# Kernel tuning notes

Hardware: AMD Instinct MI355X
Metric: run time of the kernel (lower is better)

The kernel has to match this reference:

```python
import jax, jax.numpy as jnp
import numpy as np

B, NQ, D, NH, DH = 16, 300, 256, 8, 32
L, P, FFN = 3, 4, 1024
LEVEL_SHAPES = [(80, 80), (40, 40), (20, 20)]
S = sum(h * w for h, w in LEVEL_SHAPES)  # 8400
EPS = 1e-5

PARAM_NAMES = ['wq', 'bq', 'wk', 'bk', 'wv', 'bv', 'wo', 'bo', 'ln1_g', 'ln1_b',
               'w_off', 'b_off', 'w_aw', 'b_aw', 'w_val', 'b_val', 'w_out', 'b_out',
               'ln2_g', 'ln2_b', 'w_fc1', 'b_fc1', 'w_fc2', 'b_fc2', 'ln3_g', 'ln3_b']


def _ln(x, g, b):
    m = jnp.mean(x, -1, keepdims=True)
    v = jnp.mean(jnp.square(x - m), -1, keepdims=True)
    return (x - m) * jax.lax.rsqrt(v + EPS) * g + b


def _bilinear(v_l, loc, Hl, Wl):
    # v_l: [B, Hl*Wl, NH, DH]; loc in [0,1]: [B, NQ, NH, P, 2]
    # matches torch grid_sample(align_corners=False, padding='zeros') with grid=2*loc-1
    x = loc[..., 0] * Wl - 0.5
    y = loc[..., 1] * Hl - 0.5
    x0 = jnp.floor(x)
    y0 = jnp.floor(y)
    vt = v_l.transpose(0, 2, 1, 3)  # [B, NH, Sl, DH]
    out = jnp.zeros((v_l.shape[0], NQ, NH, P, DH), v_l.dtype)
    for dx in (0, 1):
        for dy in (0, 1):
            xi = x0 + dx
            yi = y0 + dy
            w = (1.0 - jnp.abs(x - xi)) * (1.0 - jnp.abs(y - yi))
            valid = (xi >= 0) & (xi < Wl) & (yi >= 0) & (yi < Hl)
            idx = (jnp.clip(yi, 0, Hl - 1) * Wl + jnp.clip(xi, 0, Wl - 1)).astype(jnp.int32)
            idx_t = idx.transpose(0, 2, 1, 3).reshape(idx.shape[0], NH, NQ * P)
            g = jnp.take_along_axis(vt, idx_t[..., None], axis=2)  # [B, NH, NQ*P, DH]
            g = g.reshape(-1, NH, NQ, P, DH).transpose(0, 2, 1, 3, 4)
            out = out + g * (w * valid)[..., None]
    return out  # [B, NQ, NH, P, DH]


def _forward(hidden_states, pos_embed, encoder_hidden_states, reference_points, spatial_shapes, p):
    h = hidden_states
    # ---- self-attention (pos added to q and k only) ----
    hp = h + pos_embed
    q = (hp @ p['wq'] + p['bq']).reshape(B, NQ, NH, DH)
    k = (hp @ p['wk'] + p['bk']).reshape(B, NQ, NH, DH)
    v = (h @ p['wv'] + p['bv']).reshape(B, NQ, NH, DH)
    scores = jnp.einsum('bqhd,bkhd->bhqk', q, k) * (1.0 / np.sqrt(DH).astype(np.float32))
    attn = jax.nn.softmax(scores, -1)
    sa = jnp.einsum('bhqk,bkhd->bqhd', attn, v).reshape(B, NQ, D) @ p['wo'] + p['bo']
    h = _ln(h + sa, p['ln1_g'], p['ln1_b'])

    # ---- multiscale deformable cross-attention ----
    hp = h + pos_embed
    value = (encoder_hidden_states @ p['w_val'] + p['b_val']).reshape(B, S, NH, DH)
    off = (hp @ p['w_off'] + p['b_off']).reshape(B, NQ, NH, L, P, 2)
    aw = jax.nn.softmax((hp @ p['w_aw'] + p['b_aw']).reshape(B, NQ, NH, L * P), -1)
    aw = aw.reshape(B, NQ, NH, L, P)
    normalizer = jnp.stack([spatial_shapes[:, 1], spatial_shapes[:, 0]], -1).astype(h.dtype)  # [L,2] = (W,H)
    loc = reference_points[:, :, None, :, None, :] + off / normalizer[None, None, None, :, None, :]
    out = jnp.zeros((B, NQ, NH, DH), h.dtype)
    start = 0
    for l, (Hl, Wl) in enumerate(LEVEL_SHAPES):
        v_l = value[:, start:start + Hl * Wl]
        sampled = _bilinear(v_l, loc[:, :, :, l], Hl, Wl)  # [B,NQ,NH,P,DH]
        out = out + jnp.sum(sampled * aw[:, :, :, l, :, None], axis=3)
        start += Hl * Wl
    ca = out.reshape(B, NQ, D) @ p['w_out'] + p['b_out']
    h = _ln(h + ca, p['ln2_g'], p['ln2_b'])

    # ---- MLP ----
    mlp = jax.nn.relu(h @ p['w_fc1'] + p['b_fc1']) @ p['w_fc2'] + p['b_fc2']
    return _ln(h + mlp, p['ln3_g'], p['ln3_b'])


def setup_inputs() -> dict:
    key = jax.random.key(0)
    ks = iter(jax.random.split(key, 48))
    def nrm(shape, s=0.02):
        return jax.random.normal(next(ks), shape, jnp.float32) * s
    inp = {
        'hidden_states': jax.random.normal(next(ks), (B, NQ, D), jnp.float32),
        'pos_embed': jax.random.normal(next(ks), (B, NQ, D), jnp.float32),
        'encoder_hidden_states': jax.random.normal(next(ks), (B, S, D), jnp.float32),
        'reference_points': jax.random.uniform(next(ks), (B, NQ, L, 2), jnp.float32),
        'spatial_shapes': jnp.array(LEVEL_SHAPES, jnp.int32),
        'wq': nrm((D, D)), 'bq': jnp.zeros(D),
        'wk': nrm((D, D)), 'bk': jnp.zeros(D),
        'wv': nrm((D, D)), 'bv': jnp.zeros(D),
        'wo': nrm((D, D)), 'bo': jnp.zeros(D),
        'ln1_g': jnp.ones(D), 'ln1_b': jnp.zeros(D),
        'w_off': nrm((D, NH * L * P * 2)), 'b_off': nrm((NH * L * P * 2,), 0.1),
        'w_aw': nrm((D, NH * L * P)), 'b_aw': jnp.zeros(NH * L * P),
        'w_val': nrm((D, D)), 'b_val': jnp.zeros(D),
        'w_out': nrm((D, D)), 'b_out': jnp.zeros(D),
        'ln2_g': jnp.ones(D), 'ln2_b': jnp.zeros(D),
        'w_fc1': nrm((D, FFN)), 'b_fc1': jnp.zeros(FFN),
        'w_fc2': nrm((FFN, D)), 'b_fc2': jnp.zeros(D),
        'ln3_g': jnp.ones(D), 'ln3_b': jnp.zeros(D),
    }
    return inp


def reference(hidden_states, pos_embed, encoder_hidden_states, reference_points, spatial_shapes,
              wq, bq, wk, bk, wv, bv, wo, bo, ln1_g, ln1_b,
              w_off, b_off, w_aw, b_aw, w_val, b_val, w_out, b_out,
              ln2_g, ln2_b, w_fc1, b_fc1, w_fc2, b_fc2, ln3_g, ln3_b):
    p = dict(wq=wq, bq=bq, wk=wk, bk=bk, wv=wv, bv=bv, wo=wo, bo=bo,
             ln1_g=ln1_g, ln1_b=ln1_b, w_off=w_off, b_off=b_off, w_aw=w_aw, b_aw=b_aw,
             w_val=w_val, b_val=b_val, w_out=w_out, b_out=b_out, ln2_g=ln2_g, ln2_b=ln2_b,
             w_fc1=w_fc1, b_fc1=b_fc1, w_fc2=w_fc2, b_fc2=b_fc2, ln3_g=ln3_g, ln3_b=ln3_b)
    return _forward(hidden_states, pos_embed, encoder_hidden_states, reference_points, spatial_shapes, p)
```

## Files before the change

### kernel.cpp

```cpp
#include <hip/hip_runtime.h>
#include <hip/hip_bf16.h>
#include <math.h>

#define B_   16
#define NQ_  300
#define D_   256
#define NH_  8
#define DH_  32
#define L_   3
#define P_   4
#define FFN_ 1024
#define S_   8400
#define ROWS_ (B_*NQ_)
#define NB_   (ROWS_*D_)

typedef __attribute__((ext_vector_type(4))) unsigned short ushort4_t;
typedef __attribute__((ext_vector_type(8))) unsigned short ushort8_t;
typedef __attribute__((ext_vector_type(8))) short bf16x8;
typedef __attribute__((ext_vector_type(4))) float f32x4;

__device__ inline unsigned short f2b(float f) {
    __hip_bfloat16 h = __float2bfloat16(f);
    return __builtin_bit_cast(unsigned short, h);
}
__device__ inline float b2f(unsigned short u) {
    union { unsigned u; float f; } c; c.u = ((unsigned)u) << 16; return c.f;
}

__global__ __launch_bounds__(256) void prep_kernel(
    const float* __restrict__ wq, const float* __restrict__ wk,
    const float* __restrict__ wv, const float* __restrict__ wo,
    const float* __restrict__ w_val, const float* __restrict__ w_out,
    const float* __restrict__ w_off, const float* __restrict__ w_aw,
    const float* __restrict__ w_fc1, const float* __restrict__ w_fc2,
    const float* __restrict__ bq, const float* __restrict__ bk,
    const float* __restrict__ b_off, const float* __restrict__ b_aw,
    unsigned short* __restrict__ wtqk, unsigned short* __restrict__ wtv,
    unsigned short* __restrict__ wto, unsigned short* __restrict__ wtval,
    unsigned short* __restrict__ wtout, unsigned short* __restrict__ wtoa,
    unsigned short* __restrict__ wtfc1, unsigned short* __restrict__ wtfc2,
    float* __restrict__ bqk, float* __restrict__ boa)
{
    const int bid = blockIdx.x;
    if (bid >= 968) {
        int idx = (bid - 968)*256 + threadIdx.x;
        if (idx < 512) bqk[idx] = (idx < 256) ? bq[idx] : bk[idx-256];
        else { int j = idx - 512; if (j < 288) boa[j] = (j < 192) ? b_off[j] : b_aw[j-192]; }
        return;
    }
    const float* src; unsigned short* dst; int K, N, t;
    if      (bid < 64)  { src=wq;    dst=wtqk;         K=256;  N=256;  t=bid; }
    else if (bid < 128) { src=wk;    dst=wtqk+65536;   K=256;  N=256;  t=bid-64; }
    else if (bid < 192) { src=wv;    dst=wtv;          K=256;  N=256;  t=bid-128; }
    else if (bid < 256) { src=wo;    dst=wto;          K=256;  N=256;  t=bid-192; }
    else if (bid < 320) { src=w_val; dst=wtval;        K=256;  N=256;  t=bid-256; }
    else if (bid < 384) { src=w_out; dst=wtout;        K=256;  N=256;  t=bid-320; }
    else if (bid < 432) { src=w_off; dst=wtoa;         K=256;  N=192;  t=bid-384; }
    else if (bid < 456) { src=w_aw;  dst=wtoa+49152;   K=256;  N=96;   t=bid-432; }
    else if (bid < 712) { src=w_fc1; dst=wtfc1;        K=256;  N=1024; t=bid-456; }
    else                { src=w_fc2; dst=wtfc2;        K=1024; N=256;  t=bid-712; }

    __shared__ unsigned short tl[32][33];
    int tid = threadIdx.x;
    int tx = tid & 31, ty = tid >> 5;
    int ntx = N >> 5;
    int n0 = (t % ntx) * 32, k0 = (t / ntx) * 32;
    #pragma unroll
    for (int i = 0; i < 4; ++i)
        tl[tx][ty + i*8] = f2b(src[(size_t)(k0 + ty + i*8)*N + n0 + tx]);
    __syncthreads();
    #pragma unroll
    for (int i = 0; i < 4; ++i)
        dst[(size_t)(n0 + ty + i*8)*K + k0 + tx] = tl[ty + i*8][tx];
}

#define GEMM_PREAMBLE()                                                        \
    const int tid  = threadIdx.x;                                              \
    const int lane = tid & 63;                                                 \
    const int w    = tid >> 6;                                                 \
    const int wr   = w >> 1, wc = w & 1;                                       \
    const int m0   = blockIdx.y * 64;                                          \
    const int n0   = blockIdx.x * 128;                                         \
    const int fr   = lane & 15, fq = lane >> 4;                                \
    const int arow = tid >> 2, aseg = (tid & 3) * 8;                           \
    const int brow = tid >> 1, bseg = (tid & 1) * 16;                          \
    const bool a_ok = (m0 + arow) < M;                                         \
    const bool b_ok = (n0 + brow) < N;                                         \
    const float*          aptr  = A  + (size_t)(m0 + arow)*K + aseg;           \
    const float*          aptr2 = A2 ? A2 + (size_t)(m0 + arow)*K + aseg : (const float*)0; \
    const unsigned short* bptr  = WT + (size_t)(n0 + brow)*K + bseg;           \
    f32x4 acc[2][4];                                                           \
    _Pragma("unroll") for (int m = 0; m < 2; ++m)                              \
        _Pragma("unroll") for (int n = 0; n < 4; ++n)                          \
            acc[m][n] = (f32x4){0.f, 0.f, 0.f, 0.f};                           \
    float4 avA0, avB0, avA1, avB1;                                             \
    ushort8_t bvA0, bvB0, bvA1, bvB1;

#define GEMM_LOAD(avA, avB, bvA, bvB, kk) do {                                 \
    if (a_ok) {                                                                \
        avA = *(const float4*)(aptr + (kk));                                   \
        avB = *(const float4*)(aptr + (kk) + 4);                               \
        if (aptr2) {                                                           \
            float4 x2 = *(const float4*)(aptr2 + (kk));                        \
            float4 y2 = *(const float4*)(aptr2 + (kk) + 4);                    \
            avA.x += x2.x; avA.y += x2.y; avA.z += x2.z; avA.w += x2.w;        \
            avB.x += y2.x; avB.y += y2.y; avB.z += y2.z; avB.w += y2.w;        \
        }                                                                      \
    } else { avA = (float4){0,0,0,0}; avB = (float4){0,0,0,0}; }               \
    if (b_ok) { bvA = *(const ushort8_t*)(bptr + (kk));                        \
                bvB = *(const ushort8_t*)(bptr + (kk) + 8); }                  \
    else { _Pragma("unroll") for (int j = 0; j < 8; ++j){bvA[j]=0;bvB[j]=0;} } \
} while (0)

#define GEMM_STORE_LDS(avA, avB, bvA, bvB) do {                                \
    ushort8_t ac;                                                              \
    ac[0]=f2b(avA.x); ac[1]=f2b(avA.y); ac[2]=f2b(avA.z); ac[3]=f2b(avA.w);    \
    ac[4]=f2b(avB.x); ac[5]=f2b(avB.y); ac[6]=f2b(avB.z); ac[7]=f2b(avB.w);    \
    *(ushort8_t*)&As[arow][aseg]     = ac;                                     \
    *(ushort8_t*)&Bs[brow][bseg]     = bvA;                                    \
    *(ushort8_t*)&Bs[brow][bseg + 8] = bvB;                                    \
} while (0)

#define GEMM_COMPUTE() do {                                                    \
    bf16x8 af[2], bfv[4];                                                      \
    _Pragma("unroll") for (int m = 0; m < 2; ++m)                              \
        af[m] = *(const bf16x8*)&As[wr*32 + m*16 + fr][fq*8];                  \
    _Pragma("unroll") for (int n = 0; n < 4; ++n)                              \
        bfv[n] = *(const bf16x8*)&Bs[wc*64 + n*16 + fr][fq*8];                 \
    _Pragma("unroll") for (int m = 0; m < 2; ++m)                              \
        _Pragma("unroll") for (int n = 0; n < 4; ++n)                          \
            acc[m][n] = __builtin_amdgcn_mfma_f32_16x16x32_bf16(               \
                af[m], bfv[n], acc[m][n], 0, 0, 0);                            \
} while (0)

#define GEMM_KLOOP()                                                           \
    GEMM_LOAD(avA0, avB0, bvA0, bvB0, 0);                                      \
    for (int k0 = 0; k0 < K; k0 += 64) {                                       \
        __syncthreads();                                                       \
        GEMM_STORE_LDS(avA0, avB0, bvA0, bvB0);                                \
        GEMM_LOAD(avA1, avB1, bvA1, bvB1, k0 + 32);                            \
        __syncthreads();                                                       \
        GEMM_COMPUTE();                                                        \
        __syncthreads();                                                       \
        GEMM_STORE_LDS(avA1, avB1, bvA1, bvB1);                                \
        if (k0 + 64 < K) GEMM_LOAD(avA0, avB0, bvA0, bvB0, k0 + 64);           \
        __syncthreads();                                                       \
        GEMM_COMPUTE();                                                        \
    }

__global__ __launch_bounds__(256) void gemm_mfma64(
    const float* __restrict__ A, const float* __restrict__ A2,
    const unsigned short* __restrict__ WT,
    const float* __restrict__ bias, float* __restrict__ C,
    int M, int N, int K, int relu)
{
    __shared__ unsigned short As[64][40];
    __shared__ unsigned short Bs[128][40];
    GEMM_PREAMBLE();
    GEMM_KLOOP();

    #pragma unroll
    for (int n = 0; n < 4; ++n) {
        int col = n0 + wc*64 + n*16 + fr;
        if (col < N) {
            float bcol = bias[col];
            #pragma unroll
            for (int m = 0; m < 2; ++m) {
                int rbase = m0 + wr*32 + m*16 + fq*4;
                #pragma unroll
                for (int r = 0; r < 4; ++r) {
                    int row = rbase + r;
                    if (row < M) {
                        float vv = acc[m][n][r] + bcol;
                        if (relu) vv = fmaxf(vv, 0.f);
                        C[(size_t)row * N + col] = vv;
                    }
                }
            }
        }
    }
}

__global__ __launch_bounds__(256) void stage1_kernel(
    const float* __restrict__ ehs, const float* __restrict__ h_in,
    const float* __restrict__ pos,
    const unsigned short* __restrict__ wtval, const float* __restrict__ b_val,
    unsigned short* __restrict__ val_bf,
    const unsigned short* __restrict__ wtqk, const float* __restrict__ bqk,
    float* __restrict__ buf_qk,
    const unsigned short* __restrict__ wtv, const float* __restrict__ bv,
    float* __restrict__ buf_v)
{
    __shared__ unsigned short As[64][40];
    __shared__ unsigned short Bs[128][40];

    const int bid = blockIdx.x;
    int path, m0, n0, Ncols = 256;
    const float* Ap; const float* A2p = nullptr;
    const unsigned short* Bp; const float* bias; float* C = nullptr;
    if (bid < 4200) {
        path = 0; m0 = (bid >> 1)*64; n0 = (bid & 1)*128;
        Ap = ehs; Bp = wtval; bias = b_val;
    } else if (bid < 4500) {
        int t = bid - 4200;
        path = 1; m0 = (t >> 2)*64; n0 = (t & 3)*128;
        Ap = h_in; A2p = pos; Bp = wtqk; bias = bqk; C = buf_qk; Ncols = 512;
    } else {
        int t = bid - 4500;
        path = 2; m0 = (t >> 1)*64; n0 = (t & 1)*128;
        Ap = h_in; Bp = wtv; bias = bv; C = buf_v;
    }

    const int tid  = threadIdx.x;
    const int lane = tid & 63;
    const int w    = tid >> 6;
    const int wr   = w >> 1, wc = w & 1;
    const int fr   = lane & 15, fq = lane >> 4;
    const int arow = tid >> 2, aseg = (tid & 3) * 8;
    const int brow = tid >> 1, bseg = (tid & 1) * 16;
    const bool a_ok = true, b_ok = true;
    const int K = 256;
    const float*          aptr  = Ap + (size_t)(m0 + arow)*256 + aseg;
    const float*          aptr2 = A2p ? A2p + (size_t)(m0 + arow)*256 + aseg : (const float*)0;
    const unsigned short* bptr  = Bp + (size_t)(n0 + brow)*256 + bseg;

    f32x4 acc[2][4];
    #pragma unroll
    for (int m = 0; m < 2; ++m)
        #pragma unroll
        for (int n = 0; n < 4; ++n)
            acc[m][n] = (f32x4){0.f, 0.f, 0.f, 0.f};
    float4 avA0, avB0, avA1, avB1;
    ushort8_t bvA0, bvB0, bvA1, bvB1;

    GEMM_KLOOP();

    if (path == 0) {
        #pragma unroll
        for (int n = 0; n < 4; ++n) {
            int col = n0 + wc*64 + n*16 + fr;
            int hh = col >> 5, dd = col & 31;
            float bcol = bias[col];
            #pragma unroll
            for (int m = 0; m < 2; ++m) {
                int rbase = m0 + wr*32 + m*16 + fq*4;
                #pragma unroll
                for (int r = 0; r < 4; ++r) {
                    unsigned row = rbase + r;
                    unsigned bb = row / (unsigned)S_;
                    unsigned ss = row - bb * (unsigned)S_;
                    val_bf[((size_t)(bb*NH_ + hh)*S_ + ss)*DH_ + dd] = f2b(acc[m][n][r] + bcol);
                }
            }
        }
    } else {
        #pragma unroll
        for (int n = 0; n < 4; ++n) {
            int col = n0 + wc*64 + n*16 + fr;
            float bcol = bias[col];
            #pragma unroll
            for (int m = 0; m < 2; ++m) {
                int rbase = m0 + wr*32 + m*16 + fq*4;
                #pragma unroll
                for (int r = 0; r < 4; ++r)
                    C[(size_t)(rbase + r) * Ncols + col] = acc[m][n][r] + bcol;
            }
        }
    }
}

__global__ __launch_bounds__(256) void gemm_relu_bf16(
    const float* __restrict__ A, const unsigned short* __restrict__ WT,
    const float* __restrict__ bias, unsigned short* __restrict__ OUT,
    int M, int N, int K)
{
    __shared__ unsigned short As[64][40];
    __shared__ unsigned short Bs[128][40];
    const float* A2 = nullptr;
    GEMM_PREAMBLE();
    GEMM_KLOOP();

    #pragma unroll
    for (int n = 0; n < 4; ++n) {
        int col = n0 + wc*64 + n*16 + fr;
        float bcol = bias[col];
        #pragma unroll
        for (int m = 0; m < 2; ++m) {
            int rbase = m0 + wr*32 + m*16 + fq*4;
            #pragma unroll
            for (int r = 0; r < 4; ++r)
                OUT[(size_t)(rbase + r) * N + col] = f2b(fmaxf(acc[m][n][r] + bcol, 0.f));
        }
    }
}

#define GLN_COMPUTE()  do {                                                    \
    bf16x8 af[2], bfv[8];                                                      \
    _Pragma("unroll") for (int m = 0; m < 2; ++m)                              \
        af[m] = *(const bf16x8*)&As[wr*32 + m*16 + fr][fq*8];                  \
    _Pragma("unroll") for (int n = 0; n < 8; ++n)                              \
        bfv[n] = *(const bf16x8*)&Bs[wc*128 + n*16 + fr][fq*8];                \
    _Pragma("unroll") for (int m = 0; m < 2; ++m)                              \
        _Pragma("unroll") for (int n = 0; n < 8; ++n)                          \
            acc[m][n] = __builtin_amdgcn_mfma_f32_16x16x32_bf16(               \
                af[m], bfv[n], acc[m][n], 0, 0, 0);                            \
} while (0)

#define GLN_EPILOGUE()                                                         \
    float gcol[8], bcol2[8], biascol[8];                                       \
    _Pragma("unroll") for (int n = 0; n < 8; ++n) {                            \
        int col = wc*128 + n*16 + fr;                                          \
        biascol[n] = bias[col]; gcol[n] = g[col]; bcol2[n] = bb[col];          \
    }                                                                          \
    _Pragma("unroll") for (int m = 0; m < 2; ++m) {                            \
        _Pragma("unroll") for (int r = 0; r < 4; ++r) {                        \
            int lrow = wr*32 + m*16 + fq*4 + r;                                \
            float s = 0.f, sq = 0.f;                                           \
            _Pragma("unroll") for (int n = 0; n < 8; ++n) {                    \
                float vv = acc[m][n][r] + biascol[n]                           \
                         + X[(size_t)(m0 + lrow)*256 + wc*128 + n*16 + fr];    \
                acc[m][n][r] = vv; s += vv; sq += vv*vv;                       \
            }                                                                  \
            s  += __shfl_xor(s, 1);  sq += __shfl_xor(sq, 1);                  \
            s  += __shfl_xor(s, 2);  sq += __shfl_xor(sq, 2);                  \
            s  += __shfl_xor(s, 4);  sq += __shfl_xor(sq, 4);                  \
            s  += __shfl_xor(s, 8);  sq += __shfl_xor(sq, 8);                  \
            if (fr == 0) { psum[lrow][wc] = s; psq[lrow][wc] = sq; }           \
        }                                                                      \
    }                                                                          \
    __syncthreads();                                                           \
    _Pragma("unroll") for (int m = 0; m < 2; ++m) {                            \
        _Pragma("unroll") for (int r = 0; r < 4; ++r) {                        \
            int lrow = wr*32 + m*16 + fq*4 + r;                                \
            float mean = (psum[lrow][0] + psum[lrow][1]) * (1.0f/256.0f);      \
            float ex2  = (psq[lrow][0]  + psq[lrow][1])  * (1.0f/256.0f);      \
            float rstd = rsqrtf(ex2 - mean*mean + 1e-5f);                      \
            _Pragma("unroll") for (int n = 0; n < 8; ++n) {                    \
                int col = wc*128 + n*16 + fr;                                  \
                OUT[(size_t)(m0 + lrow)*256 + col] =                           \
                    (acc[m][n][r] - mean)*rstd*gcol[n] + bcol2[n];             \
            }                                                                  \
        }                                                                      \
    }

__global__ __launch_bounds__(256) void gemm_ln_f32A(
    const float* __restrict__ A, const unsigned short* __restrict__ WT,
    const float* __restrict__ bias, const float* __restrict__ X,
    const float* __restrict__ g, const float* __restrict__ bb,
    float* __restrict__ OUT, int K)
{
    __shared__ unsigned short As[64][40];
    __shared__ unsigned short Bs[256][40];
    __shared__ float psum[64][2], psq[64][2];

    const int tid  = threadIdx.x;
    const int lane = tid & 63;
    const int w    = tid >> 6;
    const int wr   = w >> 1, wc = w & 1;
    const int m0   = blockIdx.x * 64;
    const int fr   = lane & 15, fq = lane >> 4;
    const int arow = tid >> 2, aseg = (tid & 3) * 8;
    const float*          aptr = A  + (size_t)(m0 + arow)*K + aseg;
    const unsigned short* bptr = WT + (size_t)tid*K;

    f32x4 acc[2][8];
    #pragma unroll
    for (int m = 0; m < 2; ++m)
        #pragma unroll
        for (int n = 0; n < 8; ++n)
            acc[m][n] = (f32x4){0.f, 0.f, 0.f, 0.f};

    float4 a0x, a0y, a1x, a1y;
    ushort8_t b0[4], b1[4];

    a0x = *(const float4*)(aptr); a0y = *(const float4*)(aptr + 4);
    #pragma unroll
    for (int j = 0; j < 4; ++j) b0[j] = *(const ushort8_t*)(bptr + j*8);
    for (int k0 = 0; k0 < K; k0 += 64) {
        __syncthreads();
        {
            ushort8_t ac;
            ac[0]=f2b(a0x.x); ac[1]=f2b(a0x.y); ac[2]=f2b(a0x.z); ac[3]=f2b(a0x.w);
            ac[4]=f2b(a0y.x); ac[5]=f2b(a0y.y); ac[6]=f2b(a0y.z); ac[7]=f2b(a0y.w);
            *(ushort8_t*)&As[arow][aseg] = ac;
            #pragma unroll
            for (int j = 0; j < 4; ++j) *(ushort8_t*)&Bs[tid][j*8] = b0[j];
        }
        a1x = *(const float4*)(aptr + k0 + 32); a1y = *(const float4*)(aptr + k0 + 36);
        #pragma unroll
        for (int j = 0; j < 4; ++j) b1[j] = *(const ushort8_t*)(bptr + k0 + 32 + j*8);
        __syncthreads();
        GLN_COMPUTE();
        __syncthreads();
        {
            ushort8_t ac;
            ac[0]=f2b(a1x.x); ac[1]=f2b(a1x.y); ac[2]=f2b(a1x.z); ac[3]=f2b(a1x.w);
            ac[4]=f2b(a1y.x); ac[5]=f2b(a1y.y); ac[6]=f2b(a1y.z); ac[7]=f2b(a1y.w);
            *(ushort8_t*)&As[arow][aseg] = ac;
            #pragma unroll
            for (int j = 0; j < 4; ++j) *(ushort8_t*)&Bs[tid][j*8] = b1[j];
        }
        if (k0 + 64 < K) {
            a0x = *(const float4*)(aptr + k0 + 64); a0y = *(const float4*)(aptr + k0 + 68);
            #pragma unroll
            for (int j = 0; j < 4; ++j) b0[j] = *(const ushort8_t*)(bptr + k0 + 64 + j*8);
        }
        __syncthreads();
        GLN_COMPUTE();
    }

    GLN_EPILOGUE();
}

__global__ __launch_bounds__(256) void gemm_ln_bf16A(
    const unsigned short* __restrict__ A, const unsigned short* __restrict__ WT,
    const float* __restrict__ bias, const float* __restrict__ X,
    const float* __restrict__ g, const float* __restrict__ bb,
    float* __restrict__ OUT, int K)
{
    __shared__ unsigned short As[64][40];
    __shared__ unsigned short Bs[256][40];
    __shared__ float psum[64][2], psq[64][2];

    const int tid  = threadIdx.x;
    const int lane = tid & 63;
    const int w    = tid >> 6;
    const int wr   = w >> 1, wc = w & 1;
    const int m0   = blockIdx.x * 64;
    const int fr   = lane & 15, fq = lane >> 4;
    const int arow = tid >> 2, aseg = (tid & 3) * 8;
    const unsigned short* aptr = A  + (size_t)(m0 + arow)*K + aseg;
    const unsigned short* bptr = WT + (size_t)tid*K;

    f32x4 acc[2][8];
    #pragma unroll
    for (int m = 0; m < 2; ++m)
        #pragma unroll
        for (int n = 0; n < 8; ++n)
            acc[m][n] = (f32x4){0.f, 0.f, 0.f, 0.f};

    ushort8_t a0, a1, b0[4], b1[4];

    a0 = *(const ushort8_t*)(aptr);
    #pragma unroll
    for (int j = 0; j < 4; ++j) b0[j] = *(const ushort8_t*)(bptr + j*8);
    for (int k0 = 0; k0 < K; k0 += 64) {
        __syncthreads();
        *(ushort8_t*)&As[arow][aseg] = a0;
        #pragma unroll
        for (int j = 0; j < 4; ++j) *(ushort8_t*)&Bs[tid][j*8] = b0[j];
        a1 = *(const ushort8_t*)(aptr + k0 + 32);
        #pragma unroll
        for (int j = 0; j < 4; ++j) b1[j] = *(const ushort8_t*)(bptr + k0 + 32 + j*8);
        __syncthreads();
        GLN_COMPUTE();
        __syncthreads();
        *(ushort8_t*)&As[arow][aseg] = a1;
        #pragma unroll
        for (int j = 0; j < 4; ++j) *(ushort8_t*)&Bs[tid][j*8] = b1[j];
        if (k0 + 64 < K) {
            a0 = *(const ushort8_t*)(aptr + k0 + 64);
            #pragma unroll
            for (int j = 0; j < 4; ++j) b0[j] = *(const ushort8_t*)(bptr + k0 + 64 + j*8);
        }
        __syncthreads();
        GLN_COMPUTE();
    }

    GLN_EPILOGUE();
}

__global__ __launch_bounds__(256) void self_attn_kernel(
    const float* __restrict__ qk, const float* __restrict__ v,
    float* __restrict__ sa)
{
    __shared__ unsigned short k_sw[304*32];
    __shared__ unsigned short vt[32][312];
    __shared__ unsigned short p_all[4][16][312];

    const int bid  = blockIdx.x;
    const int part = bid % 5;
    const int bh   = bid / 5;
    const int h    = bh & 7;
    const int b    = bh >> 3;
    const int tid  = threadIdx.x;
    const int lane = tid & 63;
    const int w    = tid >> 6;
    const int g    = lane >> 4;
    const int fr   = lane & 15;

    const size_t qbase = (size_t)b*NQ_*512 + h*DH_;
    const size_t kbase = qbase + 256;
    const size_t vbase = (size_t)b*NQ_*D_ + h*DH_;
    const size_t sbase = (size_t)b*NQ_*D_ + h*DH_;

    for (int i = tid; i < 1216; i += 256) {
        int r = i >> 2, u = i & 3;
        ushort8_t kb;
        if (r < NQ_) {
            const float* p8 = qk + kbase + (size_t)r*512 + u*8;
            float4 a0 = *(const float4*)p8;
            float4 a1 = *(const float4*)(p8 + 4);
            kb[0]=f2b(a0.x); kb[1]=f2b(a0.y); kb[2]=f2b(a0.z); kb[3]=f2b(a0.w);
            kb[4]=f2b(a1.x); kb[5]=f2b(a1.y); kb[6]=f2b(a1.z); kb[7]=f2b(a1.w);
        } else {
            #pragma unroll
            for (int j = 0; j < 8; ++j) kb[j] = 0;
        }
        int su = u ^ ((r >> 1) & 3);
        *(ushort8_t*)&k_sw[r*32 + su*8] = kb;
    }
    for (int i = tid; i < 1216; i += 256) {
        int kk = i >> 2, u = i & 3;
        if (kk < NQ_) {
            const float* p8 = v + vbase + (size_t)kk*D_ + u*8;
            float4 a0 = *(const float4*)p8;
            float4 a1 = *(const float4*)(p8 + 4);
            float f[8] = {a0.x,a0.y,a0.z,a0.w,a1.x,a1.y,a1.z,a1.w};
            #pragma unroll
            for (int j = 0; j < 8; ++j) vt[u*8 + j][kk] = f2b(f[j]);
        } else {
            #pragma unroll
            for (int j = 0; j < 8; ++j) vt[u*8 + j][kk] = 0;
        }
    }
    __syncthreads();

    const int q0 = part*64 + w*16;
    const int qi = q0 + fr;
    bf16x8 qf;
    if (qi < NQ_) {
        const float scale = 0.17677669529663687f;
        const float* p8 = qk + qbase + (size_t)qi*512 + g*8;
        float4 a0 = *(const float4*)p8;
        float4 a1 = *(const float4*)(p8 + 4);
        qf[0]=(short)f2b(a0.x*scale); qf[1]=(short)f2b(a0.y*scale);
        qf[2]=(short)f2b(a0.z*scale); qf[3]=(short)f2b(a0.w*scale);
        qf[4]=(short)f2b(a1.x*scale); qf[5]=(short)f2b(a1.y*scale);
        qf[6]=(short)f2b(a1.z*scale); qf[7]=(short)f2b(a1.w*scale);
    } else {
        #pragma unroll
        for (int j = 0; j < 8; ++j) qf[j] = 0;
    }

    const int ksw_u = g ^ ((fr >> 1) & 3);
    f32x4 acc[19];
    #pragma unroll
    for (int t = 0; t < 19; ++t) acc[t] = (f32x4){0.f,0.f,0.f,0.f};
    #pragma unroll
    for (int t = 0; t < 19; ++t) {
        int row = t*16 + fr;
        bf16x8 kf = *(const bf16x8*)&k_sw[row*32 + ksw_u*8];
        acc[t] = __builtin_amdgcn_mfma_f32_16x16x32_bf16(kf, qf, acc[t], 0, 0, 0);
    }
    if (g == 3) acc[18] = (f32x4){-1e30f, -1e30f, -1e30f, -1e30f};

    float m = -1e30f;
    #pragma unroll
    for (int t = 0; t < 19; ++t) {
        #pragma unroll
        for (int r = 0; r < 4; ++r) m = fmaxf(m, acc[t][r]);
    }
    m = fmaxf(m, __shfl_xor(m, 16));
    m = fmaxf(m, __shfl_xor(m, 32));
    float lsum = 0.f;
    #pragma unroll
    for (int t = 0; t < 19; ++t) {
        #pragma unroll
        for (int r = 0; r < 4; ++r) {
            float e = __expf(acc[t][r] - m);
            acc[t][r] = e;
            lsum += e;
        }
    }
    lsum += __shfl_xor(lsum, 16);
    lsum += __shfl_xor(lsum, 32);
    float inv = 1.0f / lsum;

    #pragma unroll
    for (int t = 0; t < 19; ++t) {
        ushort4_t pw = { f2b(acc[t][0]*inv), f2b(acc[t][1]*inv),
                         f2b(acc[t][2]*inv), f2b(acc[t][3]*inv) };
        *(ushort4_t*)&p_all[w][fr][t*16 + g*4] = pw;
    }

    f32x4 o0 = (f32x4){0.f,0.f,0.f,0.f};
    f32x4 o1 = (f32x4){0.f,0.f,0.f,0.f};
    #pragma unroll
    for (int ks = 0; ks < 10; ++ks) {
        int kb = ks*32 + g*8;
        bf16x8 pf, vf0, vf1;
        if (kb < 304) {
            pf  = *(const bf16x8*)&p_all[w][fr][kb];
            vf0 = *(const bf16x8*)&vt[fr][kb];
            vf1 = *(const bf16x8*)&vt[16 + fr][kb];
        } else {
            #pragma unroll
            for (int j = 0; j < 8; ++j) { pf[j] = 0; vf0[j] = 0; vf1[j] = 0; }
        }
        o0 = __builtin_amdgcn_mfma_f32_16x16x32_bf16(pf, vf0, o0, 0, 0, 0);
        o1 = __builtin_amdgcn_mfma_f32_16x16x32_bf16(pf, vf1, o1, 0, 0, 0);
    }

    #pragma unroll
    for (int r = 0; r < 4; ++r) {
        int qo = q0 + g*4 + r;
        if (qo < NQ_) {
            sa[sbase + (size_t)qo*D_ + fr]      = o0[r];
            sa[sbase + (size_t)qo*D_ + 16 + fr] = o1[r];
        }
    }
}

__global__ __launch_bounds__(256) void deform_kernel(
    const unsigned short* __restrict__ value, const float* __restrict__ oa,
    const float* __restrict__ refp, float* __restrict__ dout)
{
    int gid = blockIdx.x*256 + threadIdx.x;
    int d = gid & 31;
    int h = (gid >> 5) & 7;
    int bq = gid >> 8;
    int qq = bq % NQ_;
    int b  = bq / NQ_;

    const int starts[3] = {0, 6400, 8000};
    const int Hs[3] = {80, 40, 20};

    const float* offp = oa + (size_t)(b*NQ_+qq)*288 + h*24;
    const float* awp  = oa + (size_t)(b*NQ_+qq)*288 + 192 + h*12;
    const float* refq = refp + (size_t)(b*NQ_+qq)*(L_*2);
    const unsigned short* vb = value + ((size_t)(b*NH_ + h)*S_)*DH_ + d;

    float av[12];
    float mx = -1e30f;
    #pragma unroll
    for (int i = 0; i < 12; ++i) { av[i] = awp[i]; mx = fmaxf(mx, av[i]); }
    float ssum = 0.f;
    #pragma unroll
    for (int i = 0; i < 12; ++i) { av[i] = __expf(av[i]-mx); ssum += av[i]; }
    float sinv = 1.f / ssum;

    float acc = 0.f;
    #pragma unroll
    for (int l = 0; l < L_; l++) {
        int Hl = Hs[l], Wl = Hs[l];
        float rx = refq[l*2+0], ry = refq[l*2+1];
        const unsigned short* vlb = vb + (size_t)starts[l]*DH_;
        #pragma unroll
        for (int p = 0; p < P_; p++) {
            float ox = offp[(l*P_+p)*2+0], oy = offp[(l*P_+p)*2+1];
            float a  = av[l*P_+p] * sinv;
            float x = (rx + ox/(float)Wl)*(float)Wl - 0.5f;
            float y = (ry + oy/(float)Hl)*(float)Hl - 0.5f;
            float x0 = floorf(x), y0 = floorf(y);
            #pragma unroll
            for (int dy = 0; dy < 2; dy++) {
                #pragma unroll
                for (int dx = 0; dx < 2; dx++) {
                    float xi = x0 + dx, yi = y0 + dy;
                    float wgt = (1.f - fabsf(x-xi))*(1.f - fabsf(y-yi));
                    bool valid = (xi >= 0.f) && (xi < (float)Wl) && (yi >= 0.f) && (yi < (float)Hl);
                    if (valid && wgt != 0.f) {
                        int ix = (int)xi, iy = (int)yi;
                        acc += a * wgt * b2f(vlb[(size_t)(iy*Wl + ix)*DH_]);
                    }
                }
            }
        }
    }
    dout[gid] = acc;
}

extern "C" void kernel_launch(void* const* d_in, const int* in_sizes, int n_in,
                              void* d_out, int out_size, void* d_ws, size_t ws_size,
                              hipStream_t stream) {
    (void)in_sizes; (void)n_in; (void)out_size; (void)ws_size;
    const float* h_in  = (const float*)d_in[0];
    const float* pos   = (const float*)d_in[1];
    const float* ehs   = (const float*)d_in[2];
    const float* refp  = (const float*)d_in[3];
    const float* wq    = (const float*)d_in[5];
    const float* bq    = (const float*)d_in[6];
    const float* wk    = (const float*)d_in[7];
    const float* bk    = (const float*)d_in[8];
    const float* wv    = (const float*)d_in[9];
    const float* bv    = (const float*)d_in[10];
    const float* wo    = (const float*)d_in[11];
    const float* bo    = (const float*)d_in[12];
    const float* ln1g  = (const float*)d_in[13];
    const float* ln1b  = (const float*)d_in[14];
    const float* w_off = (const float*)d_in[15];
    const float* b_off = (const float*)d_in[16];
    const float* w_aw  = (const float*)d_in[17];
    const float* b_aw  = (const float*)d_in[18];
    const float* w_val = (const float*)d_in[19];
    const float* b_val = (const float*)d_in[20];
    const float* w_out = (const float*)d_in[21];
    const float* b_out = (const float*)d_in[22];
    const float* ln2g  = (const float*)d_in[23];
    const float* ln2b  = (const float*)d_in[24];
    const float* w_fc1 = (const float*)d_in[25];
    const float* b_fc1 = (const float*)d_in[26];
    const float* w_fc2 = (const float*)d_in[27];
    const float* b_fc2 = (const float*)d_in[28];
    const float* ln3g  = (const float*)d_in[29];
    const float* ln3b  = (const float*)d_in[30];
    float* out = (float*)d_out;

    float* ws = (float*)d_ws;
    float* buf_qk   = ws + 1*(size_t)NB_;
    float* buf_v    = ws + 3*(size_t)NB_;
    float* buf_sa   = ws + 4*(size_t)NB_;
    float* buf_h1   = ws + 6*(size_t)NB_;
    float* buf_h2   = ws + 7*(size_t)NB_;
    float* buf_oa   = ws + 8*(size_t)NB_;
    unsigned short* fc1_bf = (unsigned short*)(ws + 9*(size_t)NB_ + NB_/2);
    unsigned short* val_bf = (unsigned short*)(ws + 13*(size_t)NB_ + NB_/2);

    unsigned short* wtb = (unsigned short*)(ws + 27*(size_t)NB_ + NB_/2);
    unsigned short* wtqk  = wtb;
    unsigned short* wtv   = wtqk  + 131072;
    unsigned short* wto   = wtv   + 65536;
    unsigned short* wtval = wto   + 65536;
    unsigned short* wtout = wtval + 65536;
    unsigned short* wtoa  = wtout + 65536;
    unsigned short* wtfc1 = wtoa  + 73728;
    unsigned short* wtfc2 = wtfc1 + 262144;
    float* bqk = (float*)(wtfc2 + 262144);
    float* boa = bqk + 512;

    dim3 blk(256);

    prep_kernel<<<dim3(972), blk, 0, stream>>>(
        wq, wk, wv, wo, w_val, w_out, w_off, w_aw, w_fc1, w_fc2,
        bq, bk, b_off, b_aw,
        wtqk, wtv, wto, wtval, wtout, wtoa, wtfc1, wtfc2, bqk, boa);

    stage1_kernel<<<dim3(4650), blk, 0, stream>>>(
        ehs, h_in, pos, wtval, b_val, val_bf, wtqk, bqk, buf_qk, wtv, bv, buf_v);

    self_attn_kernel<<<dim3(B_*NH_*5), blk, 0, stream>>>(buf_qk, buf_v, buf_sa);
    gemm_ln_f32A<<<dim3(ROWS_/64), blk, 0, stream>>>(
        buf_sa, wto, bo, h_in, ln1g, ln1b, buf_h1, 256);
    gemm_mfma64<<<dim3(3, 75), blk, 0, stream>>>(buf_h1, pos, wtoa, boa, buf_oa, ROWS_, 288, D_, 0);
    deform_kernel<<<dim3(NB_/256), blk, 0, stream>>>(val_bf, buf_oa, refp, buf_v);
    gemm_ln_f32A<<<dim3(ROWS_/64), blk, 0, stream>>>(
        buf_v, wtout, b_out, buf_h1, ln2g, ln2b, buf_h2, 256);
    gemm_relu_bf16<<<dim3(8, 75), blk, 0, stream>>>(buf_h2, wtfc1, b_fc1, fc1_bf, ROWS_, FFN_, D_);
    gemm_ln_bf16A<<<dim3(ROWS_/64), blk, 0, stream>>>(
        fc1_bf, wtfc2, b_fc2, buf_h2, ln3g, ln3b, out, FFN_);
}
```

Baseline: 231.1 us.

## Shrink GEMM+LayerNorm row tiles to 16 and pair channels in deform sampling

```diff
diff --git a/kernel.cpp b/kernel.cpp
--- a/kernel.cpp
+++ b/kernel.cpp
@@ -294,52 +294,45 @@
     }
 }
 
-#define GLN_COMPUTE()  do {                                                    \
-    bf16x8 af[2], bfv[8];                                                      \
-    _Pragma("unroll") for (int m = 0; m < 2; ++m)                              \
-        af[m] = *(const bf16x8*)&As[wr*32 + m*16 + fr][fq*8];                  \
-    _Pragma("unroll") for (int n = 0; n < 8; ++n)                              \
-        bfv[n] = *(const bf16x8*)&Bs[wc*128 + n*16 + fr][fq*8];                \
-    _Pragma("unroll") for (int m = 0; m < 2; ++m)                              \
-        _Pragma("unroll") for (int n = 0; n < 8; ++n)                          \
-            acc[m][n] = __builtin_amdgcn_mfma_f32_16x16x32_bf16(               \
-                af[m], bfv[n], acc[m][n], 0, 0, 0);                            \
+#define GLN16_COMPUTE() do {                                                   \
+    bf16x8 af = *(const bf16x8*)&As[fr][fq*8];                                 \
+    _Pragma("unroll") for (int n = 0; n < 4; ++n) {                            \
+        bf16x8 bfv = *(const bf16x8*)&Bs[w*64 + n*16 + fr][fq*8];              \
+        acc[n] = __builtin_amdgcn_mfma_f32_16x16x32_bf16(af, bfv, acc[n], 0, 0, 0); \
+    }                                                                          \
 } while (0)
 
-#define GLN_EPILOGUE()                                                         \
-    float gcol[8], bcol2[8], biascol[8];                                       \
-    _Pragma("unroll") for (int n = 0; n < 8; ++n) {                            \
-        int col = wc*128 + n*16 + fr;                                          \
+#define GLN16_EPILOGUE()                                                       \
+    float gcol[4], bcol2[4], biascol[4];                                       \
+    _Pragma("unroll") for (int n = 0; n < 4; ++n) {                            \
+        int col = w*64 + n*16 + fr;                                            \
         biascol[n] = bias[col]; gcol[n] = g[col]; bcol2[n] = bb[col];          \
     }                                                                          \
-    _Pragma("unroll") for (int m = 0; m < 2; ++m) {                            \
-        _Pragma("unroll") for (int r = 0; r < 4; ++r) {                        \
-            int lrow = wr*32 + m*16 + fq*4 + r;                                \
-            float s = 0.f, sq = 0.f;                                           \
-            _Pragma("unroll") for (int n = 0; n < 8; ++n) {                    \
-                float vv = acc[m][n][r] + biascol[n]                           \
-                         + X[(size_t)(m0 + lrow)*256 + wc*128 + n*16 + fr];    \
-                acc[m][n][r] = vv; s += vv; sq += vv*vv;                       \
-            }                                                                  \
-            s  += __shfl_xor(s, 1);  sq += __shfl_xor(sq, 1);                  \
-            s  += __shfl_xor(s, 2);  sq += __shfl_xor(sq, 2);                  \
-            s  += __shfl_xor(s, 4);  sq += __shfl_xor(sq, 4);                  \
-            s  += __shfl_xor(s, 8);  sq += __shfl_xor(sq, 8);                  \
-            if (fr == 0) { psum[lrow][wc] = s; psq[lrow][wc] = sq; }           \
+    _Pragma("unroll") for (int r = 0; r < 4; ++r) {                            \
+        int row = fq*4 + r;                                                    \
+        float s = 0.f, sq = 0.f;                                               \
+        _Pragma("unroll") for (int n = 0; n < 4; ++n) {                        \
+            int col = w*64 + n*16 + fr;                                        \
+            float vv = acc[n][r] + biascol[n]                                  \
+                     + X[(size_t)(m0 + row)*256 + col];                        \
+            acc[n][r] = vv; s += vv; sq += vv*vv;                              \
         }                                                                      \
+        s  += __shfl_xor(s, 1);  sq += __shfl_xor(sq, 1);                      \
+        s  += __shfl_xor(s, 2);  sq += __shfl_xor(sq, 2);                      \
+        s  += __shfl_xor(s, 4);  sq += __shfl_xor(sq, 4);                      \
+        s  += __shfl_xor(s, 8);  sq += __shfl_xor(sq, 8);                      \
+        if (fr == 0) { psum[row][w] = s; psq[row][w] = sq; }                   \
     }                                                                          \
     __syncthreads();                                                           \
-    _Pragma("unroll") for (int m = 0; m < 2; ++m) {                            \
-        _Pragma("unroll") for (int r = 0; r < 4; ++r) {                        \
-            int lrow = wr*32 + m*16 + fq*4 + r;                                \
-            float mean = (psum[lrow][0] + psum[lrow][1]) * (1.0f/256.0f);      \
-            float ex2  = (psq[lrow][0]  + psq[lrow][1])  * (1.0f/256.0f);      \
-            float rstd = rsqrtf(ex2 - mean*mean + 1e-5f);                      \
-            _Pragma("unroll") for (int n = 0; n < 8; ++n) {                    \
-                int col = wc*128 + n*16 + fr;                                  \
-                OUT[(size_t)(m0 + lrow)*256 + col] =                           \
-                    (acc[m][n][r] - mean)*rstd*gcol[n] + bcol2[n];             \
-            }                                                                  \
+    _Pragma("unroll") for (int r = 0; r < 4; ++r) {                            \
+        int row = fq*4 + r;                                                    \
+        float mean = (psum[row][0]+psum[row][1]+psum[row][2]+psum[row][3]) * (1.0f/256.0f); \
+        float ex2  = (psq[row][0]+psq[row][1]+psq[row][2]+psq[row][3]) * (1.0f/256.0f);     \
+        float rstd = rsqrtf(ex2 - mean*mean + 1e-5f);                          \
+        _Pragma("unroll") for (int n = 0; n < 4; ++n) {                        \
+            int col = w*64 + n*16 + fr;                                        \
+            OUT[(size_t)(m0 + row)*256 + col] =                                \
+                (acc[n][r] - mean)*rstd*gcol[n] + bcol2[n];                    \
         }                                                                      \
     }
 
@@ -349,67 +342,64 @@
     const float* __restrict__ g, const float* __restrict__ bb,
     float* __restrict__ OUT, int K)
 {
-    __shared__ unsigned short As[64][40];
+    __shared__ unsigned short As[16][40];
     __shared__ unsigned short Bs[256][40];
-    __shared__ float psum[64][2], psq[64][2];
+    __shared__ float psum[16][4], psq[16][4];
 
     const int tid  = threadIdx.x;
     const int lane = tid & 63;
     const int w    = tid >> 6;
-    const int wr   = w >> 1, wc = w & 1;
-    const int m0   = blockIdx.x * 64;
+    const int m0   = blockIdx.x * 16;
     const int fr   = lane & 15, fq = lane >> 4;
-    const int arow = tid >> 2, aseg = (tid & 3) * 8;
+    const bool astage = tid < 64;
+    const int arow = (tid >> 2) & 15, aseg = (tid & 3) * 8;
     const float*          aptr = A  + (size_t)(m0 + arow)*K + aseg;
     const unsigned short* bptr = WT + (size_t)tid*K;
 
-    f32x4 acc[2][8];
-    #pragma unroll
-    for (int m = 0; m < 2; ++m)
-        #pragma unroll
-        for (int n = 0; n < 8; ++n)
-            acc[m][n] = (f32x4){0.f, 0.f, 0.f, 0.f};
-
-    float4 a0x, a0y, a1x, a1y;
+    f32x4 acc[4];
+    #pragma unroll
+    for (int n = 0; n < 4; ++n) acc[n] = (f32x4){0.f, 0.f, 0.f, 0.f};
+
+    float4 a0x = {0,0,0,0}, a0y = {0,0,0,0}, a1x = {0,0,0,0}, a1y = {0,0,0,0};
     ushort8_t b0[4], b1[4];
 
-    a0x = *(const float4*)(aptr); a0y = *(const float4*)(aptr + 4);
+    if (astage) { a0x = *(const float4*)(aptr); a0y = *(const float4*)(aptr + 4); }
     #pragma unroll
     for (int j = 0; j < 4; ++j) b0[j] = *(const ushort8_t*)(bptr + j*8);
     for (int k0 = 0; k0 < K; k0 += 64) {
         __syncthreads();
-        {
+        if (astage) {
             ushort8_t ac;
             ac[0]=f2b(a0x.x); ac[1]=f2b(a0x.y); ac[2]=f2b(a0x.z); ac[3]=f2b(a0x.w);
             ac[4]=f2b(a0y.x); ac[5]=f2b(a0y.y); ac[6]=f2b(a0y.z); ac[7]=f2b(a0y.w);
             *(ushort8_t*)&As[arow][aseg] = ac;
-            #pragma unroll
-            for (int j = 0; j < 4; ++j) *(ushort8_t*)&Bs[tid][j*8] = b0[j];
-        }
-        a1x = *(const float4*)(aptr + k0 + 32); a1y = *(const float4*)(aptr + k0 + 36);
+        }
+        #pragma unroll
+        for (int j = 0; j < 4; ++j) *(ushort8_t*)&Bs[tid][j*8] = b0[j];
+        if (astage) { a1x = *(const float4*)(aptr + k0 + 32); a1y = *(const float4*)(aptr + k0 + 36); }
         #pragma unroll
         for (int j = 0; j < 4; ++j) b1[j] = *(const ushort8_t*)(bptr + k0 + 32 + j*8);
         __syncthreads();
-        GLN_COMPUTE();
+        GLN16_COMPUTE();
         __syncthreads();
-        {
+        if (astage) {
             ushort8_t ac;
             ac[0]=f2b(a1x.x); ac[1]=f2b(a1x.y); ac[2]=f2b(a1x.z); ac[3]=f2b(a1x.w);
             ac[4]=f2b(a1y.x); ac[5]=f2b(a1y.y); ac[6]=f2b(a1y.z); ac[7]=f2b(a1y.w);
             *(ushort8_t*)&As[arow][aseg] = ac;
-            #pragma unroll
-            for (int j = 0; j < 4; ++j) *(ushort8_t*)&Bs[tid][j*8] = b1[j];
-        }
+        }
+        #pragma unroll
+        for (int j = 0; j < 4; ++j) *(ushort8_t*)&Bs[tid][j*8] = b1[j];
         if (k0 + 64 < K) {
-            a0x = *(const float4*)(aptr + k0 + 64); a0y = *(const float4*)(aptr + k0 + 68);
+            if (astage) { a0x = *(const float4*)(aptr + k0 + 64); a0y = *(const float4*)(aptr + k0 + 68); }
             #pragma unroll
             for (int j = 0; j < 4; ++j) b0[j] = *(const ushort8_t*)(bptr + k0 + 64 + j*8);
         }
         __syncthreads();
-        GLN_COMPUTE();
-    }
-
-    GLN_EPILOGUE();
+        GLN16_COMPUTE();
+    }
+
+    GLN16_EPILOGUE();
 }
 
 __global__ __launch_bounds__(256) void gemm_ln_bf16A(
@@ -418,56 +408,55 @@
     const float* __restrict__ g, const float* __restrict__ bb,
     float* __restrict__ OUT, int K)
 {
-    __shared__ unsigned short As[64][40];
+    __shared__ unsigned short As[16][40];
     __shared__ unsigned short Bs[256][40];
-    __shared__ float psum[64][2], psq[64][2];
+    __shared__ float psum[16][4], psq[16][4];
 
     const int tid  = threadIdx.x;
     const int lane = tid & 63;
     const int w    = tid >> 6;
-    const int wr   = w >> 1, wc = w & 1;
-    const int m0   = blockIdx.x * 64;
+    const int m0   = blockIdx.x * 16;
     const int fr   = lane & 15, fq = lane >> 4;
-    const int arow = tid >> 2, aseg = (tid & 3) * 8;
+    const bool astage = tid < 64;
+    const int arow = (tid >> 2) & 15, aseg = (tid & 3) * 8;
     const unsigned short* aptr = A  + (size_t)(m0 + arow)*K + aseg;
     const unsigned short* bptr = WT + (size_t)tid*K;
 
-    f32x4 acc[2][8];
-    #pragma unroll
-    for (int m = 0; m < 2; ++m)
-        #pragma unroll
-        for (int n = 0; n < 8; ++n)
-            acc[m][n] = (f32x4){0.f, 0.f, 0.f, 0.f};
+    f32x4 acc[4];
+    #pragma unroll
+    for (int n = 0; n < 4; ++n) acc[n] = (f32x4){0.f, 0.f, 0.f, 0.f};
 
     ushort8_t a0, a1, b0[4], b1[4];
-
-    a0 = *(const ushort8_t*)(aptr);
+    #pragma unroll
+    for (int j = 0; j < 8; ++j) { a0[j] = 0; a1[j] = 0; }
+
+    if (astage) a0 = *(const ushort8_t*)(aptr);
     #pragma unroll
     for (int j = 0; j < 4; ++j) b0[j] = *(const ushort8_t*)(bptr + j*8);
     for (int k0 = 0; k0 < K; k0 += 64) {
         __syncthreads();
-        *(ushort8_t*)&As[arow][aseg] = a0;
+        if (astage) *(ushort8_t*)&As[arow][aseg] = a0;
         #pragma unroll
         for (int j = 0; j < 4; ++j) *(ushort8_t*)&Bs[tid][j*8] = b0[j];
-        a1 = *(const ushort8_t*)(aptr + k0 + 32);
+        if (astage) a1 = *(const ushort8_t*)(aptr + k0 + 32);
         #pragma unroll
         for (int j = 0; j < 4; ++j) b1[j] = *(const ushort8_t*)(bptr + k0 + 32 + j*8);
         __syncthreads();
-        GLN_COMPUTE();
+        GLN16_COMPUTE();
         __syncthreads();
-        *(ushort8_t*)&As[arow][aseg] = a1;
+        if (astage) *(ushort8_t*)&As[arow][aseg] = a1;
         #pragma unroll
         for (int j = 0; j < 4; ++j) *(ushort8_t*)&Bs[tid][j*8] = b1[j];
         if (k0 + 64 < K) {
-            a0 = *(const ushort8_t*)(aptr + k0 + 64);
+            if (astage) a0 = *(const ushort8_t*)(aptr + k0 + 64);
             #pragma unroll
             for (int j = 0; j < 4; ++j) b0[j] = *(const ushort8_t*)(bptr + k0 + 64 + j*8);
         }
         __syncthreads();
-        GLN_COMPUTE();
-    }
-
-    GLN_EPILOGUE();
+        GLN16_COMPUTE();
+    }
+
+    GLN16_EPILOGUE();
 }
 
 __global__ __launch_bounds__(256) void self_attn_kernel(
@@ -617,11 +606,13 @@
     const float* __restrict__ refp, float* __restrict__ dout)
 {
     int gid = blockIdx.x*256 + threadIdx.x;
-    int d = gid & 31;
-    int h = (gid >> 5) & 7;
-    int bq = gid >> 8;
+    int l16 = gid & 15;
+    int grp = gid >> 4;
+    int h = grp & 7;
+    int bq = grp >> 3;
     int qq = bq % NQ_;
     int b  = bq / NQ_;
+    int d0 = l16*2;
 
     const int starts[3] = {0, 6400, 8000};
     const int Hs[3] = {80, 40, 20};
@@ -629,7 +620,7 @@
     const float* offp = oa + (size_t)(b*NQ_+qq)*288 + h*24;
     const float* awp  = oa + (size_t)(b*NQ_+qq)*288 + 192 + h*12;
     const float* refq = refp + (size_t)(b*NQ_+qq)*(L_*2);
-    const unsigned short* vb = value + ((size_t)(b*NH_ + h)*S_)*DH_ + d;
+    const unsigned short* vb = value + ((size_t)(b*NH_ + h)*S_)*DH_ + d0;
 
     float av[12];
     float mx = -1e30f;
@@ -640,7 +631,7 @@
     for (int i = 0; i < 12; ++i) { av[i] = __expf(av[i]-mx); ssum += av[i]; }
     float sinv = 1.f / ssum;
 
-    float acc = 0.f;
+    float acc0 = 0.f, acc1 = 0.f;
     #pragma unroll
     for (int l = 0; l < L_; l++) {
         int Hl = Hs[l], Wl = Hs[l];
@@ -662,13 +653,17 @@
                     bool valid = (xi >= 0.f) && (xi < (float)Wl) && (yi >= 0.f) && (yi < (float)Hl);
                     if (valid && wgt != 0.f) {
                         int ix = (int)xi, iy = (int)yi;
-                        acc += a * wgt * b2f(vlb[(size_t)(iy*Wl + ix)*DH_]);
+                        unsigned u = *(const unsigned*)(vlb + (size_t)(iy*Wl + ix)*DH_);
+                        float aw2 = a * wgt;
+                        acc0 += aw2 * b2f((unsigned short)(u & 0xffff));
+                        acc1 += aw2 * b2f((unsigned short)(u >> 16));
                     }
                 }
             }
         }
     }
-    dout[gid] = acc;
+    float2 o = { acc0, acc1 };
+    *(float2*)&dout[(size_t)grp*32 + d0] = o;
 }
 
 extern "C" void kernel_launch(void* const* d_in, const int* in_sizes, int n_in,
@@ -740,13 +735,13 @@
         ehs, h_in, pos, wtval, b_val, val_bf, wtqk, bqk, buf_qk, wtv, bv, buf_v);
 
     self_attn_kernel<<<dim3(B_*NH_*5), blk, 0, stream>>>(buf_qk, buf_v, buf_sa);
-    gemm_ln_f32A<<<dim3(ROWS_/64), blk, 0, stream>>>(
+    gemm_ln_f32A<<<dim3(ROWS_/16), blk, 0, stream>>>(
         buf_sa, wto, bo, h_in, ln1g, ln1b, buf_h1, 256);
     gemm_mfma64<<<dim3(3, 75), blk, 0, stream>>>(buf_h1, pos, wtoa, boa, buf_oa, ROWS_, 288, D_, 0);
-    deform_kernel<<<dim3(NB_/256), blk, 0, stream>>>(val_bf, buf_oa, refp, buf_v);
-    gemm_ln_f32A<<<dim3(ROWS_/64), blk, 0, stream>>>(
+    deform_kernel<<<dim3(ROWS_*NH_*16/256), blk, 0, stream>>>(val_bf, buf_oa, refp, buf_v);
+    gemm_ln_f32A<<<dim3(ROWS_/16), blk, 0, stream>>>(
         buf_v, wtout, b_out, buf_h1, ln2g, ln2b, buf_h2, 256);
     gemm_relu_bf16<<<dim3(8, 75), blk, 0, stream>>>(buf_h2, wtfc1, b_fc1, fc1_bf, ROWS_, FFN_, D_);
-    gemm_ln_bf16A<<<dim3(ROWS_/64), blk, 0, stream>>>(
+    gemm_ln_bf16A<<<dim3(ROWS_/16), blk, 0, stream>>>(
         fc1_bf, wtfc2, b_fc2, buf_h2, ln3g, ln3b, out, FFN_);
 }
```

Measured after the change: 216.3 us. -6.4%, faster.
